# Kernel optimization log

Hardware: AMD Instinct MI355X
Metric: run time of the kernel (lower is better)

The kernel has to match this reference:

```python
import jax, jax.numpy as jnp
import numpy as np
from jax import lax

B, S, HID = 256, 4096, 128


def setup_inputs() -> dict:
    key = jax.random.key(0)
    ks = jax.random.split(key, 11)
    return {
        "inputs": jax.random.normal(ks[0], (B, S, 3), jnp.float32),
        "hx0": jax.random.normal(ks[1], (B, HID), jnp.float32),
        "cx0": jax.random.normal(ks[2], (B, HID), jnp.float32),
        "W_inp": jax.random.normal(ks[3], (64, 3), jnp.float32) * 0.1,
        "b_inp": jax.random.normal(ks[4], (64,), jnp.float32) * 0.1,
        "W_ih": jax.random.normal(ks[5], (4 * HID, 64), jnp.float32) * 0.05,
        "b_ih": jax.random.normal(ks[6], (4 * HID,), jnp.float32) * 0.05,
        "W_hh": jax.random.normal(ks[7], (4 * HID, HID), jnp.float32) * 0.05,
        "b_hh": jax.random.normal(ks[8], (4 * HID,), jnp.float32) * 0.05,
        "W_out": jax.random.normal(ks[9], (40, HID), jnp.float32) * 0.1,
        "b_out": jax.random.normal(ks[10], (40,), jnp.float32) * 0.1,
    }


def reference(inputs, hx0, cx0, W_inp, b_inp, W_ih, b_ih, W_hh, b_hh, W_out, b_out):
    # Input projection for all steps at once (math identical to per-step Linear).
    x = jnp.einsum("bsi,hi->bsh", inputs, W_inp) + b_inp  # (B, S, 64)
    x = jnp.swapaxes(x, 0, 1)  # (S, B, 64) for scan over time

    def step(carry, x_t):
        hx, cx, _ = carry
        gates = x_t @ W_ih.T + b_ih + hx @ W_hh.T + b_hh  # (B, 4H)
        i, f, g, o = jnp.split(gates, 4, axis=-1)
        i = jax.nn.sigmoid(i)
        f = jax.nn.sigmoid(f)
        g = jnp.tanh(g)
        o = jax.nn.sigmoid(o)
        cx_new = f * cx + i * g
        hx_new = o * jnp.tanh(cx_new)
        # original: keep old hx only if ALL old hx > new hx (buggy tuple branch never taken in practice)
        hx_carry = jnp.where(jnp.all(hx > hx_new), hx, hx_new)
        return (hx_carry, cx_new, hx_new), None

    (_, _, hx_last), _ = lax.scan(step, (hx0, cx0, hx0), x)
    # Returned output is out-Linear of the last step's raw LSTM hidden state.
    return hx_last @ W_out.T + b_out  # (B, 40)
```

## Files before the change

kernel.cpp:

```cpp
#include <hip/hip_runtime.h>

#define SEQ  4096
#define HID  128
#define BT   4
#define NBLK (256 / BT)

typedef int   i32x4 __attribute__((ext_vector_type(4)));
typedef float f32x4 __attribute__((ext_vector_type(4)));

#define L2E  1.44269504088896340736f
#define L2E2 2.88539008177792681472f

__device__ __forceinline__ float exp2_(float x) { return __builtin_amdgcn_exp2f(x); }
__device__ __forceinline__ float rcp_(float x)  { return __builtin_amdgcn_rcpf(x); }
__device__ __forceinline__ float sigm2(float xp) { return rcp_(1.f + exp2_(-xp)); }
__device__ __forceinline__ float tanh2(float xp) { return 1.f - 2.f * rcp_(1.f + exp2_(xp)); }

__global__ __launch_bounds__(512, 2)
void lstm_mfma(const float* __restrict__ inputs,
               const float* __restrict__ hx0,
               const float* __restrict__ cx0,
               const float* __restrict__ W_inp,
               const float* __restrict__ b_inp,
               const float* __restrict__ W_ih,
               const float* __restrict__ b_ih,
               const float* __restrict__ W_hh,
               const float* __restrict__ b_hh,
               const float* __restrict__ W_out,
               const float* __restrict__ b_out,
               float*       __restrict__ out)
{
    __shared__ signed char xvT[2][2][4][4][16];
    __shared__ float uring[16][4][4];
    __shared__ float hxf[BT][HID + 4];

    const int tid  = threadIdx.x;
    const int w    = tid >> 6;
    const int lane = tid & 63;
    const int q    = lane >> 4;
    const int n    = lane & 15;
    const int bbase = blockIdx.x * BT;

    const int hi   = (n >> 3) & 1;
    const int b2   = (n >> 2) & 1;
    const int col  = n & 3;
    const int hrow = w * 16 + q * 4 + hi * 2 + b2;

    i32x4 A[4][2];
    float dq[4];
    #pragma unroll
    for (int t = 0; t < 4; ++t) {
        const int m = t * 128 + w * 16 + n;
        const float* whr = W_hh + m * HID;
        float mx = 0.f;
        for (int k = 0; k < 128; ++k) mx = fmaxf(mx, fabsf(whr[k]));
        const float rs = (mx > 0.f) ? 127.f / mx : 0.f;
        #pragma unroll
        for (int kt = 0; kt < 2; ++kt) {
            union { signed char c[16]; i32x4 v; } pk;
            #pragma unroll
            for (int i = 0; i < 16; ++i)
                pk.c[i] = (signed char)(int)rintf(whr[kt * 64 + q * 16 + i] * rs);
            A[t][kt] = pk.v;
        }
        const int me = t * 128 + hrow;
        const float* whe = W_hh + me * HID;
        float mxe = 0.f;
        for (int k = 0; k < 128; ++k) mxe = fmaxf(mxe, fabsf(whe[k]));
        dq[t] = (mxe / 127.f) * (1.f / 127.f) * ((t == 2) ? L2E2 : L2E);
    }

    float4 wf[4];
    #pragma unroll
    for (int t = 0; t < 4; ++t) {
        const float scl = (t == 2) ? L2E2 : L2E;
        const int m2 = t * 128 + hrow;
        const float* wir = W_ih + m2 * 64;
        float wx = 0.f, wy = 0.f, wz = 0.f, bb = 0.f;
        for (int hh = 0; hh < 64; ++hh) {
            float wv = wir[hh];
            wx += wv * W_inp[hh * 3 + 0];
            wy += wv * W_inp[hh * 3 + 1];
            wz += wv * W_inp[hh * 3 + 2];
            bb += wv * b_inp[hh];
        }
        bb += b_ih[m2] + b_hh[m2];
        wf[t] = make_float4(wx * scl, wy * scl, wz * scl, bb * scl);
    }

    const int  F0 = lane, F1 = lane + 64;
    const int  col0 = F0 / 24, rem0 = F0 % 24, slot0 = rem0 / 3, wi0 = rem0 % 3;
    const bool f1v = (F1 < 96);
    const int  col1 = f1v ? F1 / 24 : 0, rem1 = f1v ? F1 % 24 : 0;
    const int  slot1 = rem1 / 3, wi1 = rem1 % 3;
    const float* up0 = inputs + (size_t)(bbase + col0) * (SEQ * 3) + wi0;
    const float* up1 = inputs + (size_t)(bbase + col1) * (SEQ * 3) + wi1;

    for (int i = tid; i < 2 * 2 * 4 * 4 * 16; i += 512) ((signed char*)xvT)[i] = 0;
    __syncthreads();
    for (int idx = tid; idx < BT * HID; idx += 512) {
        int c = idx >> 7, h = idx & 127;
        float v = hx0[(bbase + c) * HID + h];
        v = fminf(fmaxf(v, -1.f), 1.f);
        xvT[0][h >> 6][(h >> 4) & 3][c][h & 15] = (signed char)(int)rintf(v * 127.f);
    }
    if (w == 1) {
        uring[slot0][col0][wi0]     = up0[slot0 * 3];
        uring[8 + slot0][col0][wi0] = up0[(8 + slot0) * 3];
        if (f1v) {
            uring[slot1][col1][wi1]     = up1[slot1 * 3];
            uring[8 + slot1][col1][wi1] = up1[(8 + slot1) * 3];
        }
    }
    float creg = cx0[(bbase + col) * HID + hrow];
    __syncthreads();

    const int kw = hrow >> 6, qw = (hrow >> 4) & 3, iw = hrow & 15;
    float pend0 = 0.f, pend1 = 0.f, hl = 0.f;

    for (int sb = 0; sb < SEQ; sb += 16) {
        #pragma unroll
        for (int j = 0; j < 16; ++j) {
            signed char (*br)[4][4][16] = xvT[j & 1];
            signed char (*bw)[4][4][16] = xvT[(j + 1) & 1];

            if (w == 1) {
                if (j == 0) {
                    int st0 = sb + 8 + slot0; if (st0 > SEQ - 1) st0 = SEQ - 1;
                    pend0 = up0[st0 * 3];
                    if (f1v) { int st1 = sb + 8 + slot1; if (st1 > SEQ - 1) st1 = SEQ - 1;
                               pend1 = up1[st1 * 3]; }
                } else if (j == 4) {
                    uring[8 + slot0][col0][wi0] = pend0;
                    if (f1v) uring[8 + slot1][col1][wi1] = pend1;
                } else if (j == 8) {
                    int st0 = sb + 16 + slot0; if (st0 > SEQ - 1) st0 = SEQ - 1;
                    pend0 = up0[st0 * 3];
                    if (f1v) { int st1 = sb + 16 + slot1; if (st1 > SEQ - 1) st1 = SEQ - 1;
                               pend1 = up1[st1 * 3]; }
                } else if (j == 12) {
                    uring[slot0][col0][wi0] = pend0;
                    if (f1v) uring[slot1][col1][wi1] = pend1;
                }
            }

            const f32x4 u4 = *reinterpret_cast<const f32x4*>(&uring[j][col][0]);
            const i32x4 B0 = *reinterpret_cast<const i32x4*>(&br[0][q][col][0]);
            const i32x4 B1 = *reinterpret_cast<const i32x4*>(&br[1][q][col][0]);

            float inp0 = fmaf(wf[0].x, u4[0], fmaf(wf[0].y, u4[1], fmaf(wf[0].z, u4[2], wf[0].w)));
            float inp1 = fmaf(wf[1].x, u4[0], fmaf(wf[1].y, u4[1], fmaf(wf[1].z, u4[2], wf[1].w)));
            float inp2 = fmaf(wf[2].x, u4[0], fmaf(wf[2].y, u4[1], fmaf(wf[2].z, u4[2], wf[2].w)));
            float inp3 = fmaf(wf[3].x, u4[0], fmaf(wf[3].y, u4[1], fmaf(wf[3].z, u4[2], wf[3].w)));

            const i32x4 z4 = {0, 0, 0, 0};
            __builtin_amdgcn_s_setprio(1);
            i32x4 a0 = __builtin_amdgcn_mfma_i32_16x16x64_i8(A[0][0], B0, z4, 0, 0, 0);
            a0       = __builtin_amdgcn_mfma_i32_16x16x64_i8(A[0][1], B1, a0, 0, 0, 0);
            int r0 = hi ? (b2 ? a0[3] : a0[2]) : (b2 ? a0[1] : a0[0]);
            float iv = sigm2((float)r0 * dq[0] + inp0);

            i32x4 a1 = __builtin_amdgcn_mfma_i32_16x16x64_i8(A[1][0], B0, z4, 0, 0, 0);
            a1       = __builtin_amdgcn_mfma_i32_16x16x64_i8(A[1][1], B1, a1, 0, 0, 0);
            int r1 = hi ? (b2 ? a1[3] : a1[2]) : (b2 ? a1[1] : a1[0]);
            float fv = sigm2((float)r1 * dq[1] + inp1);

            i32x4 a2 = __builtin_amdgcn_mfma_i32_16x16x64_i8(A[2][0], B0, z4, 0, 0, 0);
            a2       = __builtin_amdgcn_mfma_i32_16x16x64_i8(A[2][1], B1, a2, 0, 0, 0);
            int r2 = hi ? (b2 ? a2[3] : a2[2]) : (b2 ? a2[1] : a2[0]);
            float gv = tanh2((float)r2 * dq[2] + inp2);
            creg = fv * creg + iv * gv;
            float th = tanh2(creg * L2E2);

            i32x4 a3 = __builtin_amdgcn_mfma_i32_16x16x64_i8(A[3][0], B0, z4, 0, 0, 0);
            a3       = __builtin_amdgcn_mfma_i32_16x16x64_i8(A[3][1], B1, a3, 0, 0, 0);
            __builtin_amdgcn_s_setprio(0);
            int r3 = hi ? (b2 ? a3[3] : a3[2]) : (b2 ? a3[1] : a3[0]);
            float ov = sigm2((float)r3 * dq[3] + inp3);

            float h = ov * th;
            hl = h;
            bw[kw][qw][col][iw] = (signed char)(int)rintf(h * 127.f);
            __syncthreads();
        }
    }

    hxf[col][hrow] = hl;
    __syncthreads();
    if (tid < BT * 40) {
        int bl = tid / 40, o = tid % 40;
        const float* wr = W_out + o * HID;
        float a = b_out[o];
        #pragma unroll 8
        for (int k = 0; k < HID; ++k) a += wr[k] * hxf[bl][k];
        out[(bbase + bl) * 40 + o] = a;
    }
}

extern "C" void kernel_launch(void* const* d_in, const int* in_sizes, int n_in,
                              void* d_out, int out_size, void* d_ws, size_t ws_size,
                              hipStream_t stream) {
    const float* inputs = (const float*)d_in[0];
    const float* hx0    = (const float*)d_in[1];
    const float* cx0    = (const float*)d_in[2];
    const float* W_inp  = (const float*)d_in[3];
    const float* b_inp  = (const float*)d_in[4];
    const float* W_ih   = (const float*)d_in[5];
    const float* b_ih   = (const float*)d_in[6];
    const float* W_hh   = (const float*)d_in[7];
    const float* b_hh   = (const float*)d_in[8];
    const float* W_out  = (const float*)d_in[9];
    const float* b_out  = (const float*)d_in[10];
    float* out = (float*)d_out;

    lstm_mfma<<<NBLK, 512, 0, stream>>>(inputs, hx0, cx0, W_inp, b_inp, W_ih, b_ih,
                                        W_hh, b_hh, W_out, b_out, out);
}
```

Measured before the change: 1.684 ms.

## Halve batch per block to 2 and use 4 waves with doubled MFMA per wave

Reduces the batch tile from 4 to 2 sequences per block, doubling the block count to 128, and shrinks each block to 256 threads (4 waves). Each wave now owns two 16-row slices of W_hh per gate, so it issues twice as many int8 MFMAs per step and holds twice the A-fragment registers. The gate results are remapped so each lane still handles one (hidden row, batch column) pair. The goal is a per-step barrier across fewer waves and more blocks spread over CUs to shorten the serial recurrence. The cost is more MFMA work and register pressure per wave, and removal of the s_setprio hints.

```diff
diff --git a/kernel.cpp b/kernel.cpp
--- a/kernel.cpp
+++ b/kernel.cpp
@@ -2,7 +2,7 @@
 
 #define SEQ  4096
 #define HID  128
-#define BT   4
+#define BT   2
 #define NBLK (256 / BT)
 
 typedef int   i32x4 __attribute__((ext_vector_type(4)));
@@ -16,7 +16,7 @@
 __device__ __forceinline__ float sigm2(float xp) { return rcp_(1.f + exp2_(-xp)); }
 __device__ __forceinline__ float tanh2(float xp) { return 1.f - 2.f * rcp_(1.f + exp2_(xp)); }
 
-__global__ __launch_bounds__(512, 2)
+__global__ __launch_bounds__(256, 2)
 void lstm_mfma(const float* __restrict__ inputs,
                const float* __restrict__ hx0,
                const float* __restrict__ cx0,
@@ -30,8 +30,8 @@
                const float* __restrict__ b_out,
                float*       __restrict__ out)
 {
-    __shared__ signed char xvT[2][2][4][4][16];
-    __shared__ float uring[16][4][4];
+    __shared__ signed char xvT[2][2][4][2][16];
+    __shared__ float uring[16][2][4];
     __shared__ float hxf[BT][HID + 4];
 
     const int tid  = threadIdx.x;
@@ -41,27 +41,32 @@
     const int n    = lane & 15;
     const int bbase = blockIdx.x * BT;
 
-    const int hi   = (n >> 3) & 1;
-    const int b2   = (n >> 2) & 1;
-    const int col  = n & 3;
-    const int hrow = w * 16 + q * 4 + hi * 2 + b2;
-
-    i32x4 A[4][2];
+    const int  cc   = n & 1;
+    const bool rb1  = (n >> 1) & 1;
+    const bool rb2  = (n >> 2) & 1;
+    const bool hi8  = (n >> 3) & 1;
+    const int  rr   = (n >> 1) & 3;
+    const int  hrow = w * 16 + (hi8 ? 64 : 0) + q * 4 + rr;
+
+    i32x4 A[4][2][2];
     float dq[4];
     #pragma unroll
     for (int t = 0; t < 4; ++t) {
-        const int m = t * 128 + w * 16 + n;
-        const float* whr = W_hh + m * HID;
-        float mx = 0.f;
-        for (int k = 0; k < 128; ++k) mx = fmaxf(mx, fabsf(whr[k]));
-        const float rs = (mx > 0.f) ? 127.f / mx : 0.f;
         #pragma unroll
-        for (int kt = 0; kt < 2; ++kt) {
-            union { signed char c[16]; i32x4 v; } pk;
+        for (int s = 0; s < 2; ++s) {
+            const int m = t * 128 + (w + 4 * s) * 16 + n;
+            const float* whr = W_hh + m * HID;
+            float mx = 0.f;
+            for (int k = 0; k < 128; ++k) mx = fmaxf(mx, fabsf(whr[k]));
+            const float rs = (mx > 0.f) ? 127.f / mx : 0.f;
             #pragma unroll
-            for (int i = 0; i < 16; ++i)
-                pk.c[i] = (signed char)(int)rintf(whr[kt * 64 + q * 16 + i] * rs);
-            A[t][kt] = pk.v;
+            for (int kt = 0; kt < 2; ++kt) {
+                union { signed char c[16]; i32x4 v; } pk;
+                #pragma unroll
+                for (int i = 0; i < 16; ++i)
+                    pk.c[i] = (signed char)(int)rintf(whr[kt * 64 + q * 16 + i] * rs);
+                A[t][s][kt] = pk.v;
+            }
         }
         const int me = t * 128 + hrow;
         const float* whe = W_hh + me * HID;
@@ -88,104 +93,88 @@
         wf[t] = make_float4(wx * scl, wy * scl, wz * scl, bb * scl);
     }
 
-    const int  F0 = lane, F1 = lane + 64;
-    const int  col0 = F0 / 24, rem0 = F0 % 24, slot0 = rem0 / 3, wi0 = rem0 % 3;
-    const bool f1v = (F1 < 96);
-    const int  col1 = f1v ? F1 / 24 : 0, rem1 = f1v ? F1 % 24 : 0;
-    const int  slot1 = rem1 / 3, wi1 = rem1 % 3;
+    const bool uldr = (w == 1) && (lane < 48);
+    const int  col0 = lane / 24, rem0 = lane % 24, slot0 = rem0 / 3, wi0 = rem0 % 3;
     const float* up0 = inputs + (size_t)(bbase + col0) * (SEQ * 3) + wi0;
-    const float* up1 = inputs + (size_t)(bbase + col1) * (SEQ * 3) + wi1;
-
-    for (int i = tid; i < 2 * 2 * 4 * 4 * 16; i += 512) ((signed char*)xvT)[i] = 0;
+
+    if (tid < 2 * 2 * 4 * 2 * 16 / 4) ((int*)xvT)[tid] = 0;
     __syncthreads();
-    for (int idx = tid; idx < BT * HID; idx += 512) {
-        int c = idx >> 7, h = idx & 127;
+    {
+        int c = tid >> 7, h = tid & 127;
         float v = hx0[(bbase + c) * HID + h];
         v = fminf(fmaxf(v, -1.f), 1.f);
         xvT[0][h >> 6][(h >> 4) & 3][c][h & 15] = (signed char)(int)rintf(v * 127.f);
     }
-    if (w == 1) {
+    if (uldr) {
         uring[slot0][col0][wi0]     = up0[slot0 * 3];
         uring[8 + slot0][col0][wi0] = up0[(8 + slot0) * 3];
-        if (f1v) {
-            uring[slot1][col1][wi1]     = up1[slot1 * 3];
-            uring[8 + slot1][col1][wi1] = up1[(8 + slot1) * 3];
-        }
-    }
-    float creg = cx0[(bbase + col) * HID + hrow];
+    }
+    float creg = cx0[(bbase + cc) * HID + hrow];
     __syncthreads();
 
-    const int kw = hrow >> 6, qw = (hrow >> 4) & 3, iw = hrow & 15;
-    float pend0 = 0.f, pend1 = 0.f, hl = 0.f;
+    float pend0 = 0.f, hl = 0.f;
 
     for (int sb = 0; sb < SEQ; sb += 16) {
         #pragma unroll
         for (int j = 0; j < 16; ++j) {
-            signed char (*br)[4][4][16] = xvT[j & 1];
-            signed char (*bw)[4][4][16] = xvT[(j + 1) & 1];
-
-            if (w == 1) {
+            signed char (*br)[4][2][16] = xvT[j & 1];
+            signed char (*bw)[4][2][16] = xvT[(j + 1) & 1];
+
+            if (uldr) {
                 if (j == 0) {
                     int st0 = sb + 8 + slot0; if (st0 > SEQ - 1) st0 = SEQ - 1;
                     pend0 = up0[st0 * 3];
-                    if (f1v) { int st1 = sb + 8 + slot1; if (st1 > SEQ - 1) st1 = SEQ - 1;
-                               pend1 = up1[st1 * 3]; }
                 } else if (j == 4) {
                     uring[8 + slot0][col0][wi0] = pend0;
-                    if (f1v) uring[8 + slot1][col1][wi1] = pend1;
                 } else if (j == 8) {
                     int st0 = sb + 16 + slot0; if (st0 > SEQ - 1) st0 = SEQ - 1;
                     pend0 = up0[st0 * 3];
-                    if (f1v) { int st1 = sb + 16 + slot1; if (st1 > SEQ - 1) st1 = SEQ - 1;
-                               pend1 = up1[st1 * 3]; }
                 } else if (j == 12) {
                     uring[slot0][col0][wi0] = pend0;
-                    if (f1v) uring[slot1][col1][wi1] = pend1;
                 }
             }
 
-            const f32x4 u4 = *reinterpret_cast<const f32x4*>(&uring[j][col][0]);
-            const i32x4 B0 = *reinterpret_cast<const i32x4*>(&br[0][q][col][0]);
-            const i32x4 B1 = *reinterpret_cast<const i32x4*>(&br[1][q][col][0]);
-
-            float inp0 = fmaf(wf[0].x, u4[0], fmaf(wf[0].y, u4[1], fmaf(wf[0].z, u4[2], wf[0].w)));
-            float inp1 = fmaf(wf[1].x, u4[0], fmaf(wf[1].y, u4[1], fmaf(wf[1].z, u4[2], wf[1].w)));
-            float inp2 = fmaf(wf[2].x, u4[0], fmaf(wf[2].y, u4[1], fmaf(wf[2].z, u4[2], wf[2].w)));
-            float inp3 = fmaf(wf[3].x, u4[0], fmaf(wf[3].y, u4[1], fmaf(wf[3].z, u4[2], wf[3].w)));
+            const f32x4 u4 = *reinterpret_cast<const f32x4*>(&uring[j][cc][0]);
+            const i32x4 B0 = *reinterpret_cast<const i32x4*>(&br[0][q][cc][0]);
+            const i32x4 B1 = *reinterpret_cast<const i32x4*>(&br[1][q][cc][0]);
+
+            float inp[4];
+            #pragma unroll
+            for (int t = 0; t < 4; ++t)
+                inp[t] = fmaf(wf[t].x, u4[0], fmaf(wf[t].y, u4[1],
+                         fmaf(wf[t].z, u4[2], wf[t].w)));
 
             const i32x4 z4 = {0, 0, 0, 0};
-            __builtin_amdgcn_s_setprio(1);
-            i32x4 a0 = __builtin_amdgcn_mfma_i32_16x16x64_i8(A[0][0], B0, z4, 0, 0, 0);
-            a0       = __builtin_amdgcn_mfma_i32_16x16x64_i8(A[0][1], B1, a0, 0, 0, 0);
-            int r0 = hi ? (b2 ? a0[3] : a0[2]) : (b2 ? a0[1] : a0[0]);
-            float iv = sigm2((float)r0 * dq[0] + inp0);
-
-            i32x4 a1 = __builtin_amdgcn_mfma_i32_16x16x64_i8(A[1][0], B0, z4, 0, 0, 0);
-            a1       = __builtin_amdgcn_mfma_i32_16x16x64_i8(A[1][1], B1, a1, 0, 0, 0);
-            int r1 = hi ? (b2 ? a1[3] : a1[2]) : (b2 ? a1[1] : a1[0]);
-            float fv = sigm2((float)r1 * dq[1] + inp1);
-
-            i32x4 a2 = __builtin_amdgcn_mfma_i32_16x16x64_i8(A[2][0], B0, z4, 0, 0, 0);
-            a2       = __builtin_amdgcn_mfma_i32_16x16x64_i8(A[2][1], B1, a2, 0, 0, 0);
-            int r2 = hi ? (b2 ? a2[3] : a2[2]) : (b2 ? a2[1] : a2[0]);
-            float gv = tanh2((float)r2 * dq[2] + inp2);
-            creg = fv * creg + iv * gv;
+            float gv4[4];
+            #pragma unroll
+            for (int t = 0; t < 4; ++t) {
+                i32x4 a0 = __builtin_amdgcn_mfma_i32_16x16x64_i8(A[t][0][0], B0, z4, 0, 0, 0);
+                a0       = __builtin_amdgcn_mfma_i32_16x16x64_i8(A[t][0][1], B1, a0, 0, 0, 0);
+                i32x4 a1 = __builtin_amdgcn_mfma_i32_16x16x64_i8(A[t][1][0], B0, z4, 0, 0, 0);
+                a1       = __builtin_amdgcn_mfma_i32_16x16x64_i8(A[t][1][1], B1, a1, 0, 0, 0);
+                int s0 = rb1 ? a0[1] : a0[0];
+                int s1 = rb1 ? a0[3] : a0[2];
+                int v0 = rb2 ? s1 : s0;
+                int t0 = rb1 ? a1[1] : a1[0];
+                int t1 = rb1 ? a1[3] : a1[2];
+                int v1 = rb2 ? t1 : t0;
+                int v  = hi8 ? v1 : v0;
+                gv4[t] = (float)v * dq[t] + inp[t];
+            }
+
+            float iv = sigm2(gv4[0]), fv = sigm2(gv4[1]);
+            float gg = tanh2(gv4[2]), ov = sigm2(gv4[3]);
+            creg = fv * creg + iv * gg;
             float th = tanh2(creg * L2E2);
-
-            i32x4 a3 = __builtin_amdgcn_mfma_i32_16x16x64_i8(A[3][0], B0, z4, 0, 0, 0);
-            a3       = __builtin_amdgcn_mfma_i32_16x16x64_i8(A[3][1], B1, a3, 0, 0, 0);
-            __builtin_amdgcn_s_setprio(0);
-            int r3 = hi ? (b2 ? a3[3] : a3[2]) : (b2 ? a3[1] : a3[0]);
-            float ov = sigm2((float)r3 * dq[3] + inp3);
-
-            float h = ov * th;
+            float h  = ov * th;
             hl = h;
-            bw[kw][qw][col][iw] = (signed char)(int)rintf(h * 127.f);
+
+            bw[hi8 ? 1 : 0][w][cc][q * 4 + rr] = (signed char)(int)rintf(h * 127.f);
             __syncthreads();
         }
     }
 
-    hxf[col][hrow] = hl;
+    hxf[cc][hrow] = hl;
     __syncthreads();
     if (tid < BT * 40) {
         int bl = tid / 40, o = tid % 40;
@@ -213,6 +202,6 @@
     const float* b_out  = (const float*)d_in[10];
     float* out = (float*)d_out;
 
-    lstm_mfma<<<NBLK, 512, 0, stream>>>(inputs, hx0, cx0, W_inp, b_inp, W_ih, b_ih,
+    lstm_mfma<<<NBLK, 256, 0, stream>>>(inputs, hx0, cx0, W_inp, b_inp, W_ih, b_ih,
                                         W_hh, b_hh, W_out, b_out, out);
 }
```

New measurement: 1.464 ms (median of 2 runs). -13.0%, faster.
